# Performance work log

Measured on AMD Instinct MI355X. Metric: run time of the kernel, lower is better.

The kernel has to match this reference:

```python
import jax, jax.numpy as jnp
import numpy as np

E = 1024
M = 6
GH = 256
FR = 16  # FiLM bottleneck r = max(16, E//64)


def setup_inputs() -> dict:
    key = jax.random.key(0)
    ks = jax.random.split(key, 32)
    n = lambda k, shape, std=0.02: jax.random.normal(k, shape, dtype=jnp.float32) * std
    inp = {
        "x": jax.random.normal(ks[0], (4, 2048, E), dtype=jnp.float32),
        # gate MLP E->GH->M
        "gw1": n(ks[1], (E, GH)), "gb1": jnp.zeros((GH,), jnp.float32),
        "gw2": n(ks[2], (GH, M)), "gb2": jnp.zeros((M,), jnp.float32),
        "ebias": jnp.zeros((M,), jnp.float32),
        "pm_alpha": jnp.float32(0.5),
        # expert 0: DoubleMLP E->2E->E
        "dfc_w": n(ks[3], (E, 2 * E)), "dfc_b": jnp.zeros((2 * E,), jnp.float32),
        "dproj_w": n(ks[4], (2 * E, E)), "dproj_b": jnp.zeros((E,), jnp.float32),
        # expert 1: SingleMLP E->E->E
        "sfc_w": n(ks[5], (E, E)), "sfc_b": jnp.zeros((E,), jnp.float32),
        "sproj_w": n(ks[6], (E, E)), "sproj_b": jnp.zeros((E,), jnp.float32),
        # expert 2: rank-2 perceptron
        "p2_w": n(ks[7], (2, E)), "p2_v": n(ks[8], (2, E)),
        "p2_alpha": jnp.ones((2,), jnp.float32), "p2_b": jnp.zeros((2,), jnp.float32),
        "p2_bias": jnp.zeros((E,), jnp.float32),
        # expert 3: rank-4 perceptron
        "p4_w": n(ks[9], (4, E)), "p4_v": n(ks[10], (4, E)),
        "p4_alpha": jnp.ones((4,), jnp.float32), "p4_b": jnp.zeros((4,), jnp.float32),
        "p4_bias": jnp.zeros((E,), jnp.float32),
        # expert 4: ReGLU1D
        "rg_u": n(ks[11], (E,)), "rg_a": jnp.ones((E,), jnp.float32),
        "rg_b": jnp.zeros((1,), jnp.float32), "rg_bias": jnp.zeros((E,), jnp.float32),
        # expert 5: FiLM E->FR->2E
        "fl_dw": n(ks[12], (E, FR)), "fl_db": jnp.zeros((FR,), jnp.float32),
        "fl_uw": n(ks[13], (FR, 2 * E)), "fl_ub": jnp.zeros((2 * E,), jnp.float32),
    }
    return inp


def _gelu(x):
    return jax.nn.gelu(x, approximate=False)  # torch nn.GELU default (erf)


def _rank_n(x, w, v, alpha, b, biasvec):
    # y = biasvec + sum_i alpha_i * gelu(<w_i,x> + b_i) * v_i
    s = jnp.einsum("bse,ne->bsn", x, w) + b
    g = _gelu(s)
    return jnp.einsum("bsn,ne->bse", alpha * g, v) + biasvec


def reference(x, gw1, gb1, gw2, gb2, ebias, pm_alpha,
              dfc_w, dfc_b, dproj_w, dproj_b,
              sfc_w, sfc_b, sproj_w, sproj_b,
              p2_w, p2_v, p2_alpha, p2_b, p2_bias,
              p4_w, p4_v, p4_alpha, p4_b, p4_bias,
              rg_u, rg_a, rg_b, rg_bias,
              fl_dw, fl_db, fl_uw, fl_ub):
    # gate logits [B,S,M]; tau=1.0
    gl = _gelu(x @ gw1 + gb1) @ gw2 + gb2 + ebias
    pi = jax.nn.softmax(gl, axis=-1)
    # top_k=1 sparse weights: mask to top-1 then renormalize
    _, topi = jax.lax.top_k(pi, 1)
    mask = jax.nn.one_hot(topi[..., 0], M, dtype=pi.dtype)
    w = pi * mask
    w = w / (jnp.sum(w, axis=-1, keepdims=True) + 1e-9)

    # experts (dropout = identity in eval)
    o0 = _gelu(x @ dfc_w + dfc_b) @ dproj_w + dproj_b            # DoubleMLP
    o1 = _gelu(x @ sfc_w + sfc_b) @ sproj_w + sproj_b            # SingleMLP
    o2 = _rank_n(x, p2_w, p2_v, p2_alpha, p2_b, p2_bias)          # perc2
    o3 = _rank_n(x, p4_w, p4_v, p4_alpha, p4_b, p4_bias)          # perc4
    s = x @ rg_u + rg_b[0]                                        # ReGLU1D
    o4 = jax.nn.sigmoid(s)[..., None] * (x * rg_a) + rg_bias
    t = _gelu(x @ fl_dw + fl_db)                                  # FiLM
    gb = t @ fl_uw + fl_ub
    gamma, beta = jnp.split(gb, 2, axis=-1)
    o5 = gamma * x + beta

    all_out = jnp.stack([o0, o1, o2, o3, o4, o5], axis=-1)        # [B,S,E,M]
    mixed = jnp.sum(all_out * w[..., None, :], axis=-1)
    return pm_alpha * mixed
```

## Files before the change

### kernel.cpp

```cpp
#include <hip/hip_runtime.h>
#include <math.h>


#define E 1024
#define GH 256
#define NEXP 6
#define NTOK 8192
#define NCH 24

typedef __attribute__((ext_vector_type(8))) short bf16x8;
typedef __attribute__((ext_vector_type(4))) float f32x4;

__device__ __forceinline__ float gelu_erf(float v) {
    return 0.5f * v * (1.0f + erff(v * 0.70710678118654752440f));
}

__device__ __forceinline__ unsigned short f2bf(float f) {
    union { float f; unsigned u; } c; c.f = f;
    unsigned u = c.u;
    u += 0x7fffu + ((u >> 16) & 1u);
    return (unsigned short)(u >> 16);
}

__device__ __forceinline__ float bf2f(unsigned short h) {
    union { unsigned u; float f; } c; c.u = ((unsigned)h) << 16;
    return c.f;
}

__device__ __forceinline__ int ldso(int row, int q) {
    return row * 32 + ((q ^ ((row >> 1) & 3)) << 3);
}

__device__ __forceinline__ void glds16(const void* g, void* l) {
    __builtin_amdgcn_global_load_lds(
        (const __attribute__((address_space(1))) void*)g,
        (__attribute__((address_space(3))) void*)l, 16, 0, 0);
}

__global__ __launch_bounds__(256)
void prep_kernel(const float* __restrict__ x, unsigned short* __restrict__ xh,
                 unsigned short* __restrict__ xl,
                 const float* __restrict__ gw1, unsigned short* __restrict__ w1cat,
                 const float* __restrict__ p2_w, const float* __restrict__ p4_w,
                 const float* __restrict__ rg_u, const float* __restrict__ fl_dw,
                 unsigned short* __restrict__ w1cheap,
                 const float* __restrict__ dfc_w, unsigned short* __restrict__ dfc_wt,
                 const float* __restrict__ dproj_w, unsigned short* __restrict__ dpj_wt,
                 const float* __restrict__ sfc_w, unsigned short* __restrict__ sfc_wt,
                 const float* __restrict__ sproj_w, unsigned short* __restrict__ spj_wt) {
    __shared__ float tile[32][33];
    const int tid = threadIdx.x;
    const int tx = tid & 31, ty = tid >> 5;
    int b = blockIdx.x;
    if (b < 2048) {
        const int n4 = NTOK * E / 4;
        for (int i = b * 256 + tid; i < n4; i += 2048 * 256) {
            float4 v = reinterpret_cast<const float4*>(x)[i];
            ushort4 h, l;
            h.x = f2bf(v.x); l.x = f2bf(v.x - bf2f(h.x));
            h.y = f2bf(v.y); l.y = f2bf(v.y - bf2f(h.y));
            h.z = f2bf(v.z); l.z = f2bf(v.z - bf2f(h.z));
            h.w = f2bf(v.w); l.w = f2bf(v.w - bf2f(h.w));
            reinterpret_cast<ushort4*>(xh)[i] = h;
            reinterpret_cast<ushort4*>(xl)[i] = l;
        }
        return;
    }
    b -= 2048;
    if (b < 256) {
        const int c0 = (b & 7) * 32, r0 = (b >> 3) * 32;
#pragma unroll
        for (int i = 0; i < 4; ++i)
            tile[ty + i * 8][tx] = gw1[(size_t)(r0 + ty + i * 8) * GH + c0 + tx];
        __syncthreads();
#pragma unroll
        for (int i = 0; i < 4; ++i) {
            float v = tile[tx][ty + i * 8];
            unsigned short h = f2bf(v);
            size_t row = (size_t)(c0 + ty + i * 8) * 2048;
            w1cat[row + r0 + tx] = h;
            w1cat[row + 1024 + r0 + tx] = f2bf(v - bf2f(h));
        }
        return;
    }
    b -= 256;
    if (b < 64) {
        const int r = b;
        const int k4 = tid * 4;
        float4 v = {0.f, 0.f, 0.f, 0.f};
        if (r < 2)       v = *reinterpret_cast<const float4*>(&p2_w[r * E + k4]);
        else if (r < 6)  v = *reinterpret_cast<const float4*>(&p4_w[(r - 2) * E + k4]);
        else if (r == 6) v = *reinterpret_cast<const float4*>(&rg_u[k4]);
        else if (r < 23) {
            const int j = r - 7;
            v.x = fl_dw[(k4 + 0) * 16 + j];
            v.y = fl_dw[(k4 + 1) * 16 + j];
            v.z = fl_dw[(k4 + 2) * 16 + j];
            v.w = fl_dw[(k4 + 3) * 16 + j];
        }
        ushort4 h, l;
        h.x = f2bf(v.x); l.x = f2bf(v.x - bf2f(h.x));
        h.y = f2bf(v.y); l.y = f2bf(v.y - bf2f(h.y));
        h.z = f2bf(v.z); l.z = f2bf(v.z - bf2f(h.z));
        h.w = f2bf(v.w); l.w = f2bf(v.w - bf2f(h.w));
        *reinterpret_cast<ushort4*>(&w1cheap[r * 2048 + k4]) = h;
        *reinterpret_cast<ushort4*>(&w1cheap[r * 2048 + 1024 + k4]) = l;
        return;
    }
    b -= 64;
    const float* src; unsigned short* dst; int R, C, nbx;
    if (b < 2048)      { src = dfc_w;   dst = dfc_wt; R = 1024; C = 2048; nbx = 64; }
    else if (b < 4096) { src = dproj_w; dst = dpj_wt; R = 2048; C = 1024; nbx = 32; b -= 2048; }
    else if (b < 5120) { src = sfc_w;   dst = sfc_wt; R = 1024; C = 1024; nbx = 32; b -= 4096; }
    else               { src = sproj_w; dst = spj_wt; R = 1024; C = 1024; nbx = 32; b -= 5120; }
    const int c0 = (b % nbx) * 32, r0 = (b / nbx) * 32;
#pragma unroll
    for (int i = 0; i < 4; ++i)
        tile[ty + i * 8][tx] = src[(size_t)(r0 + ty + i * 8) * C + c0 + tx];
    __syncthreads();
#pragma unroll
    for (int i = 0; i < 4; ++i)
        dst[(size_t)(c0 + ty + i * 8) * R + r0 + tx] = f2bf(tile[tx][ty + i * 8]);
}

__global__ __launch_bounds__(256)
void gate_partial_kernel(const unsigned short* __restrict__ xh,
                         const unsigned short* __restrict__ xl,
                         const unsigned short* __restrict__ w1cat,
                         const unsigned short* __restrict__ w1cheap,
                         float* __restrict__ hp,
                         float* __restrict__ cdot) {
    __shared__ __align__(16) unsigned short As[2][128 * 32];
    __shared__ __align__(16) unsigned short Bs[2][128 * 32];
    const int tid = threadIdx.x;
    const int bid = blockIdx.x;
    const int xcd = bid & 7, slot = bid >> 3;
    const int nx = slot & 1;
    const int strip = xcd * 32 + (slot >> 1);
    const int m = strip >> 2, c2 = strip & 3;
    const int z = c2 & 1, h = c2 >> 1;
    const int t0 = m * 128, n0 = nx * 128;
    const unsigned short* A = z ? xl : xh;
    float* hpz = hp + (size_t)c2 * ((size_t)NTOK * GH);
    float* cd  = cdot + (size_t)c2 * ((size_t)NTOK * NCH);

    const int lane = tid & 63, wv = tid >> 6;
    const int wr = wv >> 1, wc = wv & 1;
    const int lm = lane & 15, q = lane >> 4;
    const int r0 = tid >> 2, gsl = tid & 3;
    const int g = gsl ^ ((r0 >> 1) & 3);
    const int lbase = wv * 512;

    const unsigned short* pa0 = A + (size_t)(t0 + r0) * E + g * 8;
    const unsigned short* pa1 = A + (size_t)(t0 + 64 + r0) * E + g * 8;
    const unsigned short* pb0 = w1cat + (size_t)(n0 + r0) * 2048 + h * 1024 + g * 8;
    const unsigned short* pb1 = w1cat + (size_t)(n0 + 64 + r0) * 2048 + h * 1024 + g * 8;
    const unsigned short* pcw = w1cheap + (size_t)(nx * 16 + lm) * 2048 + h * 1024 + q * 8;

    f32x4 acc[4][4];
#pragma unroll
    for (int s = 0; s < 4; ++s)
#pragma unroll
        for (int t = 0; t < 4; ++t) acc[s][t] = (f32x4){0.f, 0.f, 0.f, 0.f};
    f32x4 accC[2];
    accC[0] = (f32x4){0.f, 0.f, 0.f, 0.f};
    accC[1] = (f32x4){0.f, 0.f, 0.f, 0.f};

    glds16(pa0, &As[0][lbase]);
    glds16(pa1, &As[0][2048 + lbase]);
    glds16(pb0, &Bs[0][lbase]);
    glds16(pb1, &Bs[0][2048 + lbase]);
    bf16x8 cfv = *(const bf16x8*)pcw;

    int cur = 0;
    for (int k0 = 0;; k0 += 32) {
        __syncthreads();
        const int kn = k0 + 32;
        bf16x8 cfn;
        if (kn < 1024) {
            glds16(pa0 + kn, &As[cur ^ 1][lbase]);
            glds16(pa1 + kn, &As[cur ^ 1][2048 + lbase]);
            glds16(pb0 + kn, &Bs[cur ^ 1][lbase]);
            glds16(pb1 + kn, &Bs[cur ^ 1][2048 + lbase]);
            cfn = *(const bf16x8*)(pcw + kn);
        }
        bf16x8 af[4], bfr[4];
#pragma unroll
        for (int s = 0; s < 4; ++s) af[s] = *(const bf16x8*)&As[cur][ldso(wr * 64 + s * 16 + lm, q)];
#pragma unroll
        for (int t = 0; t < 4; ++t) bfr[t] = *(const bf16x8*)&Bs[cur][ldso(wc * 64 + t * 16 + lm, q)];
#pragma unroll
        for (int s = 0; s < 4; ++s)
#pragma unroll
            for (int t = 0; t < 4; ++t)
                acc[s][t] = __builtin_amdgcn_mfma_f32_16x16x32_bf16(af[s], bfr[t], acc[s][t], 0, 0, 0);
        {
            bf16x8 ac0 = wc ? af[2] : af[0];
            bf16x8 ac1 = wc ? af[3] : af[1];
            accC[0] = __builtin_amdgcn_mfma_f32_16x16x32_bf16(ac0, cfv, accC[0], 0, 0, 0);
            accC[1] = __builtin_amdgcn_mfma_f32_16x16x32_bf16(ac1, cfv, accC[1], 0, 0, 0);
        }
        if (kn >= 1024) break;
        cfv = cfn; cur ^= 1;
    }
#pragma unroll
    for (int s = 0; s < 4; ++s)
#pragma unroll
        for (int t = 0; t < 4; ++t)
#pragma unroll
            for (int rg = 0; rg < 4; ++rg) {
                int rl = wr * 64 + s * 16 + q * 4 + rg;
                int c  = wc * 64 + t * 16 + lm;
                hpz[(size_t)(t0 + rl) * GH + n0 + c] = acc[s][t][rg];
            }
    const int cc = nx * 16 + lm;
    if (cc < NCH) {
#pragma unroll
        for (int i = 0; i < 2; ++i)
#pragma unroll
            for (int rg = 0; rg < 4; ++rg) {
                int rl = wr * 64 + wc * 32 + i * 16 + q * 4 + rg;
                cd[(size_t)(t0 + rl) * NCH + cc] = accC[i][rg];
            }
    }
}

__global__ __launch_bounds__(256)
void gate_finalize_kernel(const float* __restrict__ hp,
                          const float* __restrict__ gb1, const float* __restrict__ gw2,
                          const float* __restrict__ gb2, const float* __restrict__ ebias,
                          const float* __restrict__ pm_alpha,
                          const float* __restrict__ cdot,
                          const float* __restrict__ p2_alpha, const float* __restrict__ p2_b,
                          const float* __restrict__ p4_alpha, const float* __restrict__ p4_b,
                          const float* __restrict__ rg_b, const float* __restrict__ fl_db,
                          float* __restrict__ scale, int* __restrict__ counts,
                          int* __restrict__ tlist, int* __restrict__ eid,
                          float* __restrict__ gvec) {
    __shared__ float hs[32][264];
    __shared__ float g2s[GH * NEXP];
    __shared__ int tokexp[32];
    const int tid = threadIdx.x;
    const int t0 = blockIdx.x * 32;
    const size_t HPS = (size_t)NTOK * GH;
    for (int i = tid; i < GH * NEXP; i += 256) g2s[i] = gw2[i];
#pragma unroll
    for (int i = 0; i < 8; ++i) {
        int f4 = i * 256 + tid;
        int row = f4 >> 6, c4 = (f4 & 63) * 4;
        size_t base = (size_t)(t0 + row) * GH + c4;
        float4 a = *reinterpret_cast<const float4*>(&hp[base]);
        float4 b = *reinterpret_cast<const float4*>(&hp[HPS + base]);
        float4 c = *reinterpret_cast<const float4*>(&hp[2 * HPS + base]);
        float4 d = *reinterpret_cast<const float4*>(&hp[3 * HPS + base]);
        float4 o;
        o.x = gelu_erf(a.x + b.x + c.x + d.x + gb1[c4 + 0]);
        o.y = gelu_erf(a.y + b.y + c.y + d.y + gb1[c4 + 1]);
        o.z = gelu_erf(a.z + b.z + c.z + d.z + gb1[c4 + 2]);
        o.w = gelu_erf(a.w + b.w + c.w + d.w + gb1[c4 + 3]);
        *reinterpret_cast<float4*>(&hs[row][c4]) = o;
    }
    __syncthreads();
    const int t = tid >> 3, j = tid & 7;
    float p[NEXP] = {0.f, 0.f, 0.f, 0.f, 0.f, 0.f};
#pragma unroll 8
    for (int kk = 0; kk < 32; ++kk) {
        int k = j + kk * 8;
        float hv = hs[t][k];
        const float* gr = &g2s[k * NEXP];
#pragma unroll
        for (int m = 0; m < NEXP; ++m) p[m] += hv * gr[m];
    }
#pragma unroll
    for (int m = 0; m < NEXP; ++m) {
        p[m] += __shfl_xor(p[m], 4, 64);
        p[m] += __shfl_xor(p[m], 2, 64);
        p[m] += __shfl_xor(p[m], 1, 64);
    }
    if (j == 0) {
        float L[NEXP];
#pragma unroll
        for (int m = 0; m < NEXP; ++m) L[m] = p[m] + gb2[m] + ebias[m];
        float mx = L[0]; int am = 0;
#pragma unroll
        for (int m = 1; m < NEXP; ++m) { if (L[m] > mx) { mx = L[m]; am = m; } }
        float S = 0.f;
#pragma unroll
        for (int m = 0; m < NEXP; ++m) S += expf(L[m] - mx);
        float pt = 1.f / S;
        scale[t0 + t] = pm_alpha[0] * (pt / (pt + 1e-9f));
        eid[t0 + t] = am;
        tokexp[t] = am;
    }
    __syncthreads();
    if (tid < NEXP) {
        const int e = tid;
        int cnt = 0;
#pragma unroll
        for (int i = 0; i < 32; ++i) cnt += (tokexp[i] == e);
        if (cnt) {
            int base = atomicAdd(&counts[e], cnt);
            int pos = 0;
#pragma unroll
            for (int i = 0; i < 32; ++i)
                if (tokexp[i] == e) tlist[e * NTOK + base + (pos++)] = t0 + i;
        }
    }
    const size_t CDS = (size_t)NTOK * NCH;
    for (int i = tid; i < 32 * NCH; i += 256) {
        const int tt = i / NCH, slot = i - tt * NCH;
        const int tok = t0 + tt;
        size_t idx = (size_t)tok * NCH + slot;
        float s = cdot[idx] + cdot[CDS + idx] + cdot[2 * CDS + idx] + cdot[3 * CDS + idx];
        float val;
        if (slot < 2)       val = p2_alpha[slot] * gelu_erf(s + p2_b[slot]);
        else if (slot < 6)  val = p4_alpha[slot - 2] * gelu_erf(s + p4_b[slot - 2]);
        else if (slot == 6) val = 1.f / (1.f + expf(-(s + rg_b[0])));
        else if (slot < 23) val = gelu_erf(s + fl_db[slot - 7]);
        else                val = 0.f;
        gvec[(size_t)tok * NCH + slot] = val;
    }
}

__global__ __launch_bounds__(256)
void moe_gemm1_kernel(const unsigned short* __restrict__ xh,
                      const unsigned short* __restrict__ B0, const unsigned short* __restrict__ B1,
                      const float* __restrict__ bias0, const float* __restrict__ bias1,
                      const int* __restrict__ counts, const int* __restrict__ tlist,
                      unsigned short* __restrict__ H0, unsigned short* __restrict__ H1) {
    __shared__ __align__(16) unsigned short As[2][128 * 32];
    __shared__ __align__(16) unsigned short Bs[2][128 * 32];
    __shared__ int toks[128];
    const int tid = threadIdx.x;
    const int bid = blockIdx.x;
    const int xcd = bid & 7, slot = bid >> 3;
    int z, l, nx;
    if (slot < 32) { z = 0; l = slot >> 4; nx = slot & 15; }
    else           { z = 1; l = (slot - 32) >> 3; nx = (slot - 32) & 7; }
    const int mtile = xcd + 8 * l;
    const int i0 = mtile * 128, n0 = nx * 128;
    const int N = z ? 1024 : 2048;
    const int cnt = counts[z];
    if (i0 >= cnt) return;
    const unsigned short* Bz = z ? B1 : B0;
    const float* bias = z ? bias1 : bias0;

    if (tid < 128) toks[tid] = tlist[z * NTOK + min(i0 + tid, cnt - 1)];
    __syncthreads();

    const int lane = tid & 63, wv = tid >> 6;
    const int wr = wv >> 1, wc = wv & 1;
    const int lm = lane & 15, q = lane >> 4;
    const int r0 = tid >> 2, gsl = tid & 3;
    const int g = gsl ^ ((r0 >> 1) & 3);
    const int lbase = wv * 512;

    const unsigned short* pa0 = xh + (size_t)toks[r0] * E + g * 8;
    const unsigned short* pa1 = xh + (size_t)toks[64 + r0] * E + g * 8;
    const unsigned short* pb0 = Bz + (size_t)(n0 + r0) * E + g * 8;
    const unsigned short* pb1 = Bz + (size_t)(n0 + 64 + r0) * E + g * 8;

    f32x4 acc[4][4];
#pragma unroll
    for (int s = 0; s < 4; ++s)
#pragma unroll
        for (int t = 0; t < 4; ++t) acc[s][t] = (f32x4){0.f, 0.f, 0.f, 0.f};

    glds16(pa0, &As[0][lbase]);
    glds16(pa1, &As[0][2048 + lbase]);
    glds16(pb0, &Bs[0][lbase]);
    glds16(pb1, &Bs[0][2048 + lbase]);

    int cur = 0;
    for (int k0 = 0;; k0 += 32) {
        __syncthreads();
        const int kn = k0 + 32;
        if (kn < E) {
            glds16(pa0 + kn, &As[cur ^ 1][lbase]);
            glds16(pa1 + kn, &As[cur ^ 1][2048 + lbase]);
            glds16(pb0 + kn, &Bs[cur ^ 1][lbase]);
            glds16(pb1 + kn, &Bs[cur ^ 1][2048 + lbase]);
        }
        bf16x8 af[4], bfr[4];
#pragma unroll
        for (int s = 0; s < 4; ++s) af[s] = *(const bf16x8*)&As[cur][ldso(wr * 64 + s * 16 + lm, q)];
#pragma unroll
        for (int t = 0; t < 4; ++t) bfr[t] = *(const bf16x8*)&Bs[cur][ldso(wc * 64 + t * 16 + lm, q)];
#pragma unroll
        for (int s = 0; s < 4; ++s)
#pragma unroll
            for (int t = 0; t < 4; ++t)
                acc[s][t] = __builtin_amdgcn_mfma_f32_16x16x32_bf16(af[s], bfr[t], acc[s][t], 0, 0, 0);
        if (kn >= E) break;
        cur ^= 1;
    }
    unsigned short* Hz = z ? H1 : H0;
#pragma unroll
    for (int s = 0; s < 4; ++s)
#pragma unroll
        for (int t = 0; t < 4; ++t)
#pragma unroll
            for (int rg = 0; rg < 4; ++rg) {
                int rl = wr * 64 + s * 16 + q * 4 + rg;
                int gc = n0 + wc * 64 + t * 16 + lm;
                float v = acc[s][t][rg] + bias[gc];
                Hz[(size_t)(i0 + rl) * N + gc] = f2bf(gelu_erf(v));
            }
}

__global__ __launch_bounds__(256)
void gemm2_cheap_kernel(const unsigned short* __restrict__ h1, const unsigned short* __restrict__ h2,
                        const unsigned short* __restrict__ dpj, const unsigned short* __restrict__ spj,
                        const float* __restrict__ dproj_b, const float* __restrict__ sproj_b,
                        const int* __restrict__ counts, const int* __restrict__ tlist,
                        const float* __restrict__ scale,
                        const float* __restrict__ x, const int* __restrict__ eid,
                        const float* __restrict__ gvec,
                        const float* __restrict__ p2_v, const float* __restrict__ p2_bias,
                        const float* __restrict__ p4_v, const float* __restrict__ p4_bias,
                        const float* __restrict__ rg_a, const float* __restrict__ rg_bias,
                        const float* __restrict__ fl_uw, const float* __restrict__ fl_ub,
                        float* __restrict__ out) {
    __shared__ __align__(16) unsigned short As[2][128 * 32];
    __shared__ __align__(16) unsigned short Bs[2][128 * 32];
    __shared__ int toks[128];
    const int tid = threadIdx.x;
    const int bb = blockIdx.x;
    const int lane = tid & 63;

    if (bb < 256) {
        const int xcd = bb & 7, slot = bb >> 3;
        const int z = slot >> 4;
        const int s2 = slot & 15;
        const int l = s2 >> 3, nx = s2 & 7;
        const int mtile = xcd + 8 * l;
        const int i0 = mtile * 128, n0 = nx * 128;
        const int K = z ? 1024 : 2048;
        const int cnt = counts[z];
        if (i0 >= cnt) return;
        const int rows = min(128, cnt - i0);
        const unsigned short* Az = z ? h2 : h1;
        const unsigned short* Bz = z ? spj : dpj;
        const float* bias = z ? sproj_b : dproj_b;

        if (tid < 128) toks[tid] = tlist[z * NTOK + min(i0 + tid, cnt - 1)];
        __syncthreads();

        const int wv = tid >> 6;
        const int wr = wv >> 1, wc = wv & 1;
        const int lm = lane & 15, q = lane >> 4;
        const int r0 = tid >> 2, gsl = tid & 3;
        const int g = gsl ^ ((r0 >> 1) & 3);
        const int lbase = wv * 512;

        const unsigned short* pa0 = Az + (size_t)(i0 + r0) * K + g * 8;
        const unsigned short* pa1 = Az + (size_t)(i0 + 64 + r0) * K + g * 8;
        const unsigned short* pb0 = Bz + (size_t)(n0 + r0) * K + g * 8;
        const unsigned short* pb1 = Bz + (size_t)(n0 + 64 + r0) * K + g * 8;

        f32x4 acc[4][4];
#pragma unroll
        for (int s = 0; s < 4; ++s)
#pragma unroll
            for (int t = 0; t < 4; ++t) acc[s][t] = (f32x4){0.f, 0.f, 0.f, 0.f};

        glds16(pa0, &As[0][lbase]);
        glds16(pa1, &As[0][2048 + lbase]);
        glds16(pb0, &Bs[0][lbase]);
        glds16(pb1, &Bs[0][2048 + lbase]);

        int cur = 0;
        for (int k0 = 0;; k0 += 32) {
            __syncthreads();
            const int kn = k0 + 32;
            if (kn < K) {
                glds16(pa0 + kn, &As[cur ^ 1][lbase]);
                glds16(pa1 + kn, &As[cur ^ 1][2048 + lbase]);
                glds16(pb0 + kn, &Bs[cur ^ 1][lbase]);
                glds16(pb1 + kn, &Bs[cur ^ 1][2048 + lbase]);
            }
            bf16x8 af[4], bfr[4];
#pragma unroll
            for (int s = 0; s < 4; ++s) af[s] = *(const bf16x8*)&As[cur][ldso(wr * 64 + s * 16 + lm, q)];
#pragma unroll
            for (int t = 0; t < 4; ++t) bfr[t] = *(const bf16x8*)&Bs[cur][ldso(wc * 64 + t * 16 + lm, q)];
#pragma unroll
            for (int s = 0; s < 4; ++s)
#pragma unroll
                for (int t = 0; t < 4; ++t)
                    acc[s][t] = __builtin_amdgcn_mfma_f32_16x16x32_bf16(af[s], bfr[t], acc[s][t], 0, 0, 0);
            if (kn >= K) break;
            cur ^= 1;
        }
#pragma unroll
        for (int s = 0; s < 4; ++s)
#pragma unroll
            for (int t = 0; t < 4; ++t)
#pragma unroll
                for (int rg = 0; rg < 4; ++rg) {
                    int rl = wr * 64 + s * 16 + q * 4 + rg;
                    if (rl < rows) {
                        int gc = n0 + wc * 64 + t * 16 + lm;
                        int tok = toks[rl];
                        out[(size_t)tok * E + gc] = scale[tok] * (acc[s][t][rg] + bias[gc]);
                    }
                }
        return;
    }

    const int tok = bb - 256;
    const int e = eid[tok];
    if (e < 2) return;
    const float sc = scale[tok];
    const int k4 = tid * 4;
    const float* gv = &gvec[(size_t)tok * NCH];
    float4 o;

    if (e == 2) {
        const float g0 = gv[0], g1 = gv[1];
        float4 b0 = *reinterpret_cast<const float4*>(&p2_bias[k4]);
        float4 v0 = *reinterpret_cast<const float4*>(&p2_v[k4]);
        float4 v1 = *reinterpret_cast<const float4*>(&p2_v[E + k4]);
        o.x = b0.x + g0 * v0.x + g1 * v1.x;
        o.y = b0.y + g0 * v0.y + g1 * v1.y;
        o.z = b0.z + g0 * v0.z + g1 * v1.z;
        o.w = b0.w + g0 * v0.w + g1 * v1.w;
    } else if (e == 3) {
        o = *reinterpret_cast<const float4*>(&p4_bias[k4]);
#pragma unroll
        for (int j = 0; j < 4; ++j) {
            const float gj = gv[2 + j];
            float4 vv = *reinterpret_cast<const float4*>(&p4_v[j * E + k4]);
            o.x += gj * vv.x; o.y += gj * vv.y; o.z += gj * vv.z; o.w += gj * vv.w;
        }
    } else if (e == 4) {
        const float sg = gv[6];
        float4 xv = *reinterpret_cast<const float4*>(&x[(size_t)tok * E + k4]);
        float4 av = *reinterpret_cast<const float4*>(&rg_a[k4]);
        float4 bv = *reinterpret_cast<const float4*>(&rg_bias[k4]);
        o.x = sg * xv.x * av.x + bv.x;
        o.y = sg * xv.y * av.y + bv.y;
        o.z = sg * xv.z * av.z + bv.z;
        o.w = sg * xv.w * av.w + bv.w;
    } else {
        float4 xv = *reinterpret_cast<const float4*>(&x[(size_t)tok * E + k4]);
        float4 ga = *reinterpret_cast<const float4*>(&fl_ub[k4]);
        float4 be = *reinterpret_cast<const float4*>(&fl_ub[E + k4]);
#pragma unroll
        for (int j = 0; j < 16; ++j) {
            const float tj = gv[7 + j];
            float4 ug = *reinterpret_cast<const float4*>(&fl_uw[(size_t)j * 2 * E + k4]);
            float4 ub = *reinterpret_cast<const float4*>(&fl_uw[(size_t)j * 2 * E + E + k4]);
            ga.x += tj * ug.x; ga.y += tj * ug.y; ga.z += tj * ug.z; ga.w += tj * ug.w;
            be.x += tj * ub.x; be.y += tj * ub.y; be.z += tj * ub.z; be.w += tj * ub.w;
        }
        o.x = ga.x * xv.x + be.x;
        o.y = ga.y * xv.y + be.y;
        o.z = ga.z * xv.z + be.z;
        o.w = ga.w * xv.w + be.w;
    }
    o.x *= sc; o.y *= sc; o.z *= sc; o.w *= sc;
    *reinterpret_cast<float4*>(&out[(size_t)tok * E + k4]) = o;
}

extern "C" void kernel_launch(void* const* d_in, const int* in_sizes, int n_in,
                              void* d_out, int out_size, void* d_ws, size_t ws_size,
                              hipStream_t stream) {
    const float* x        = (const float*)d_in[0];
    const float* gw1      = (const float*)d_in[1];
    const float* gb1      = (const float*)d_in[2];
    const float* gw2      = (const float*)d_in[3];
    const float* gb2      = (const float*)d_in[4];
    const float* ebias    = (const float*)d_in[5];
    const float* pm_alpha = (const float*)d_in[6];
    const float* dfc_w    = (const float*)d_in[7];
    const float* dfc_b    = (const float*)d_in[8];
    const float* dproj_w  = (const float*)d_in[9];
    const float* dproj_b  = (const float*)d_in[10];
    const float* sfc_w    = (const float*)d_in[11];
    const float* sfc_b    = (const float*)d_in[12];
    const float* sproj_w  = (const float*)d_in[13];
    const float* sproj_b  = (const float*)d_in[14];
    const float* p2_w     = (const float*)d_in[15];
    const float* p2_v     = (const float*)d_in[16];
    const float* p2_alpha = (const float*)d_in[17];
    const float* p2_b     = (const float*)d_in[18];
    const float* p2_bias  = (const float*)d_in[19];
    const float* p4_w     = (const float*)d_in[20];
    const float* p4_v     = (const float*)d_in[21];
    const float* p4_alpha = (const float*)d_in[22];
    const float* p4_b     = (const float*)d_in[23];
    const float* p4_bias  = (const float*)d_in[24];
    const float* rg_u     = (const float*)d_in[25];
    const float* rg_a     = (const float*)d_in[26];
    const float* rg_b     = (const float*)d_in[27];
    const float* rg_bias  = (const float*)d_in[28];
    const float* fl_dw    = (const float*)d_in[29];
    const float* fl_db    = (const float*)d_in[30];
    const float* fl_uw    = (const float*)d_in[31];
    const float* fl_ub    = (const float*)d_in[32];
    float* out = (float*)d_out;

    char* ws = (char*)d_ws;
    size_t off = 0;
    int*            counts = (int*)(ws + off);            off += 256;
    float*          scale  = (float*)(ws + off);          off += (size_t)NTOK * 4;
    int*            tlist  = (int*)(ws + off);            off += (size_t)NEXP * NTOK * 4;
    int*            eid    = (int*)(ws + off);            off += (size_t)NTOK * 4;
    float*          gvec   = (float*)(ws + off);          off += (size_t)NTOK * NCH * 4;
    float*          cdot   = (float*)(ws + off);          off += (size_t)4 * NTOK * NCH * 4;
    unsigned short* w1cheap= (unsigned short*)(ws + off); off += (size_t)64 * 2048 * 2;
    unsigned short* w1cat  = (unsigned short*)(ws + off); off += (size_t)GH * 2048 * 2;
    unsigned short* dfc_wt = (unsigned short*)(ws + off); off += (size_t)2048 * 1024 * 2;
    unsigned short* dpj_wt = (unsigned short*)(ws + off); off += (size_t)1024 * 2048 * 2;
    unsigned short* sfc_wt = (unsigned short*)(ws + off); off += (size_t)1024 * 1024 * 2;
    unsigned short* spj_wt = (unsigned short*)(ws + off); off += (size_t)1024 * 1024 * 2;
    unsigned short* x_hi   = (unsigned short*)(ws + off); off += (size_t)NTOK * E * 2;
    char* U = ws + off;
    unsigned short* x_lo = (unsigned short*)U;
    unsigned short* h1   = (unsigned short*)U;
    unsigned short* h2   = (unsigned short*)(U + (size_t)16 * 1024 * 1024);
    float* hp = out;

    hipMemsetAsync(counts, 0, 256, stream);
    prep_kernel<<<8512, 256, 0, stream>>>(x, x_hi, x_lo, gw1, w1cat,
                                          p2_w, p4_w, rg_u, fl_dw, w1cheap,
                                          dfc_w, dfc_wt, dproj_w, dpj_wt,
                                          sfc_w, sfc_wt, sproj_w, spj_wt);
    gate_partial_kernel<<<512, 256, 0, stream>>>(
        x_hi, x_lo, w1cat, w1cheap, hp, cdot);
    gate_finalize_kernel<<<NTOK / 32, 256, 0, stream>>>(
        hp, gb1, gw2, gb2, ebias, pm_alpha, cdot,
        p2_alpha, p2_b, p4_alpha, p4_b, rg_b, fl_db,
        scale, counts, tlist, eid, gvec);
    moe_gemm1_kernel<<<384, 256, 0, stream>>>(
        x_hi, dfc_wt, sfc_wt, dfc_b, sfc_b, counts, tlist, h1, h2);
    gemm2_cheap_kernel<<<256 + NTOK, 256, 0, stream>>>(
        h1, h2, dpj_wt, spj_wt, dproj_b, sproj_b, counts, tlist, scale,
        x, eid, gvec,
        p2_v, p2_bias, p4_v, p4_bias,
        rg_a, rg_bias, fl_uw, fl_ub, out);
    (void)in_sizes; (void)n_in; (void)out_size; (void)ws_size;
}
```

Measured before the change: 305.6 us.

## Split cheap experts into separate kernel batching tokens per expert list

Separates the fused gemm2-plus-cheap-expert launch into a dedicated GEMM2 kernel and a new cheap-expert kernel. The cheap kernel walks per-expert token lists in groups of 8, loading the expert weight vectors once per group and reusing them across tokens instead of reloading them for every token. It also replaces 8192 per-token blocks, most of which exited early, with a 2048-block grid-stride loop. The cost is an extra kernel launch, and the cheap experts now run after GEMM2 instead of alongside it, so overlap between them is lost.

```diff
diff --git a/kernel.cpp b/kernel.cpp
--- a/kernel.cpp
+++ b/kernel.cpp
@@ -409,18 +409,12 @@
 }
 
 __global__ __launch_bounds__(256)
-void gemm2_cheap_kernel(const unsigned short* __restrict__ h1, const unsigned short* __restrict__ h2,
-                        const unsigned short* __restrict__ dpj, const unsigned short* __restrict__ spj,
-                        const float* __restrict__ dproj_b, const float* __restrict__ sproj_b,
-                        const int* __restrict__ counts, const int* __restrict__ tlist,
-                        const float* __restrict__ scale,
-                        const float* __restrict__ x, const int* __restrict__ eid,
-                        const float* __restrict__ gvec,
-                        const float* __restrict__ p2_v, const float* __restrict__ p2_bias,
-                        const float* __restrict__ p4_v, const float* __restrict__ p4_bias,
-                        const float* __restrict__ rg_a, const float* __restrict__ rg_bias,
-                        const float* __restrict__ fl_uw, const float* __restrict__ fl_ub,
-                        float* __restrict__ out) {
+void moe_gemm2_kernel(const unsigned short* __restrict__ h1, const unsigned short* __restrict__ h2,
+                      const unsigned short* __restrict__ dpj, const unsigned short* __restrict__ spj,
+                      const float* __restrict__ dproj_b, const float* __restrict__ sproj_b,
+                      const int* __restrict__ counts, const int* __restrict__ tlist,
+                      const float* __restrict__ scale,
+                      float* __restrict__ out) {
     __shared__ __align__(16) unsigned short As[2][128 * 32];
     __shared__ __align__(16) unsigned short Bs[2][128 * 32];
     __shared__ int toks[128];
@@ -428,139 +422,202 @@
     const int bb = blockIdx.x;
     const int lane = tid & 63;
 
-    if (bb < 256) {
-        const int xcd = bb & 7, slot = bb >> 3;
-        const int z = slot >> 4;
-        const int s2 = slot & 15;
-        const int l = s2 >> 3, nx = s2 & 7;
-        const int mtile = xcd + 8 * l;
-        const int i0 = mtile * 128, n0 = nx * 128;
-        const int K = z ? 1024 : 2048;
-        const int cnt = counts[z];
-        if (i0 >= cnt) return;
-        const int rows = min(128, cnt - i0);
-        const unsigned short* Az = z ? h2 : h1;
-        const unsigned short* Bz = z ? spj : dpj;
-        const float* bias = z ? sproj_b : dproj_b;
-
-        if (tid < 128) toks[tid] = tlist[z * NTOK + min(i0 + tid, cnt - 1)];
+    const int xcd = bb & 7, slot = bb >> 3;
+    const int z = slot >> 4;
+    const int s2 = slot & 15;
+    const int l = s2 >> 3, nx = s2 & 7;
+    const int mtile = xcd + 8 * l;
+    const int i0 = mtile * 128, n0 = nx * 128;
+    const int K = z ? 1024 : 2048;
+    const int cnt = counts[z];
+    if (i0 >= cnt) return;
+    const int rows = min(128, cnt - i0);
+    const unsigned short* Az = z ? h2 : h1;
+    const unsigned short* Bz = z ? spj : dpj;
+    const float* bias = z ? sproj_b : dproj_b;
+
+    if (tid < 128) toks[tid] = tlist[z * NTOK + min(i0 + tid, cnt - 1)];
+    __syncthreads();
+
+    const int wv = tid >> 6;
+    const int wr = wv >> 1, wc = wv & 1;
+    const int lm = lane & 15, q = lane >> 4;
+    const int r0 = tid >> 2, gsl = tid & 3;
+    const int g = gsl ^ ((r0 >> 1) & 3);
+    const int lbase = wv * 512;
+
+    const unsigned short* pa0 = Az + (size_t)(i0 + r0) * K + g * 8;
+    const unsigned short* pa1 = Az + (size_t)(i0 + 64 + r0) * K + g * 8;
+    const unsigned short* pb0 = Bz + (size_t)(n0 + r0) * K + g * 8;
+    const unsigned short* pb1 = Bz + (size_t)(n0 + 64 + r0) * K + g * 8;
+
+    f32x4 acc[4][4];
+#pragma unroll
+    for (int s = 0; s < 4; ++s)
+#pragma unroll
+        for (int t = 0; t < 4; ++t) acc[s][t] = (f32x4){0.f, 0.f, 0.f, 0.f};
+
+    glds16(pa0, &As[0][lbase]);
+    glds16(pa1, &As[0][2048 + lbase]);
+    glds16(pb0, &Bs[0][lbase]);
+    glds16(pb1, &Bs[0][2048 + lbase]);
+
+    int cur = 0;
+    for (int k0 = 0;; k0 += 32) {
         __syncthreads();
-
-        const int wv = tid >> 6;
-        const int wr = wv >> 1, wc = wv & 1;
-        const int lm = lane & 15, q = lane >> 4;
-        const int r0 = tid >> 2, gsl = tid & 3;
-        const int g = gsl ^ ((r0 >> 1) & 3);
-        const int lbase = wv * 512;
-
-        const unsigned short* pa0 = Az + (size_t)(i0 + r0) * K + g * 8;
-        const unsigned short* pa1 = Az + (size_t)(i0 + 64 + r0) * K + g * 8;
-        const unsigned short* pb0 = Bz + (size_t)(n0 + r0) * K + g * 8;
-        const unsigned short* pb1 = Bz + (size_t)(n0 + 64 + r0) * K + g * 8;
-
-        f32x4 acc[4][4];
+        const int kn = k0 + 32;
+        if (kn < K) {
+            glds16(pa0 + kn, &As[cur ^ 1][lbase]);
+            glds16(pa1 + kn, &As[cur ^ 1][2048 + lbase]);
+            glds16(pb0 + kn, &Bs[cur ^ 1][lbase]);
+            glds16(pb1 + kn, &Bs[cur ^ 1][2048 + lbase]);
+        }
+        bf16x8 af[4], bfr[4];
+#pragma unroll
+        for (int s = 0; s < 4; ++s) af[s] = *(const bf16x8*)&As[cur][ldso(wr * 64 + s * 16 + lm, q)];
+#pragma unroll
+        for (int t = 0; t < 4; ++t) bfr[t] = *(const bf16x8*)&Bs[cur][ldso(wc * 64 + t * 16 + lm, q)];
 #pragma unroll
         for (int s = 0; s < 4; ++s)
 #pragma unroll
-            for (int t = 0; t < 4; ++t) acc[s][t] = (f32x4){0.f, 0.f, 0.f, 0.f};
-
-        glds16(pa0, &As[0][lbase]);
-        glds16(pa1, &As[0][2048 + lbase]);
-        glds16(pb0, &Bs[0][lbase]);
-        glds16(pb1, &Bs[0][2048 + lbase]);
-
-        int cur = 0;
-        for (int k0 = 0;; k0 += 32) {
-            __syncthreads();
-            const int kn = k0 + 32;
-            if (kn < K) {
-                glds16(pa0 + kn, &As[cur ^ 1][lbase]);
-                glds16(pa1 + kn, &As[cur ^ 1][2048 + lbase]);
-                glds16(pb0 + kn, &Bs[cur ^ 1][lbase]);
-                glds16(pb1 + kn, &Bs[cur ^ 1][2048 + lbase]);
-            }
-            bf16x8 af[4], bfr[4];
-#pragma unroll
-            for (int s = 0; s < 4; ++s) af[s] = *(const bf16x8*)&As[cur][ldso(wr * 64 + s * 16 + lm, q)];
-#pragma unroll
-            for (int t = 0; t < 4; ++t) bfr[t] = *(const bf16x8*)&Bs[cur][ldso(wc * 64 + t * 16 + lm, q)];
-#pragma unroll
-            for (int s = 0; s < 4; ++s)
-#pragma unroll
-                for (int t = 0; t < 4; ++t)
-                    acc[s][t] = __builtin_amdgcn_mfma_f32_16x16x32_bf16(af[s], bfr[t], acc[s][t], 0, 0, 0);
-            if (kn >= K) break;
-            cur ^= 1;
-        }
-#pragma unroll
-        for (int s = 0; s < 4; ++s)
-#pragma unroll
             for (int t = 0; t < 4; ++t)
-#pragma unroll
-                for (int rg = 0; rg < 4; ++rg) {
-                    int rl = wr * 64 + s * 16 + q * 4 + rg;
-                    if (rl < rows) {
-                        int gc = n0 + wc * 64 + t * 16 + lm;
-                        int tok = toks[rl];
-                        out[(size_t)tok * E + gc] = scale[tok] * (acc[s][t][rg] + bias[gc]);
+                acc[s][t] = __builtin_amdgcn_mfma_f32_16x16x32_bf16(af[s], bfr[t], acc[s][t], 0, 0, 0);
+        if (kn >= K) break;
+        cur ^= 1;
+    }
+#pragma unroll
+    for (int s = 0; s < 4; ++s)
+#pragma unroll
+        for (int t = 0; t < 4; ++t)
+#pragma unroll
+            for (int rg = 0; rg < 4; ++rg) {
+                int rl = wr * 64 + s * 16 + q * 4 + rg;
+                if (rl < rows) {
+                    int gc = n0 + wc * 64 + t * 16 + lm;
+                    int tok = toks[rl];
+                    out[(size_t)tok * E + gc] = scale[tok] * (acc[s][t][rg] + bias[gc]);
+                }
+            }
+}
+
+__global__ __launch_bounds__(256)
+void cheap_kernel(const int* __restrict__ counts, const int* __restrict__ tlist,
+                  const float* __restrict__ scale, const float* __restrict__ x,
+                  const float* __restrict__ gvec,
+                  const float* __restrict__ p2_v, const float* __restrict__ p2_bias,
+                  const float* __restrict__ p4_v, const float* __restrict__ p4_bias,
+                  const float* __restrict__ rg_a, const float* __restrict__ rg_bias,
+                  const float* __restrict__ fl_uw, const float* __restrict__ fl_ub,
+                  float* __restrict__ out) {
+    __shared__ int stoks[8];
+    __shared__ float ssc[8];
+    __shared__ float sgv[8][17];
+    const int tid = threadIdx.x;
+    const int k4 = tid * 4;
+    for (int s = blockIdx.x; s < 4096; s += 2048) {
+        const int e = 2 + (s & 3);
+        const int ti = s >> 2;
+        const int cnt = counts[e];
+        const int i0 = ti * 8;
+        if (i0 >= cnt) continue;
+        const int nt = min(8, cnt - i0);
+        __syncthreads();
+        if (tid < 128) {
+            const int tt = tid >> 4, sl = tid & 15;
+            const int tk = tlist[e * NTOK + min(i0 + tt, cnt - 1)];
+            if (sl == 0) { stoks[tt] = tk; ssc[tt] = scale[tk]; }
+            const int base = (e == 2) ? 0 : (e == 3) ? 2 : (e == 4) ? 6 : 7;
+            const int ng   = (e == 2) ? 2 : (e == 3) ? 4 : (e == 4) ? 1 : 16;
+            if (sl < ng) sgv[tt][sl] = gvec[(size_t)tk * NCH + base + sl];
+        }
+        __syncthreads();
+        if (e == 2) {
+            const float4 b0 = *reinterpret_cast<const float4*>(&p2_bias[k4]);
+            const float4 v0 = *reinterpret_cast<const float4*>(&p2_v[k4]);
+            const float4 v1 = *reinterpret_cast<const float4*>(&p2_v[E + k4]);
+#pragma unroll
+            for (int tt = 0; tt < 8; ++tt) {
+                if (tt < nt) {
+                    const float g0 = sgv[tt][0], g1 = sgv[tt][1], sc = ssc[tt];
+                    float4 o;
+                    o.x = (b0.x + g0 * v0.x + g1 * v1.x) * sc;
+                    o.y = (b0.y + g0 * v0.y + g1 * v1.y) * sc;
+                    o.z = (b0.z + g0 * v0.z + g1 * v1.z) * sc;
+                    o.w = (b0.w + g0 * v0.w + g1 * v1.w) * sc;
+                    *reinterpret_cast<float4*>(&out[(size_t)stoks[tt] * E + k4]) = o;
+                }
+            }
+        } else if (e == 3) {
+            const float4 b0 = *reinterpret_cast<const float4*>(&p4_bias[k4]);
+            float4 vv[4];
+#pragma unroll
+            for (int j = 0; j < 4; ++j)
+                vv[j] = *reinterpret_cast<const float4*>(&p4_v[j * E + k4]);
+#pragma unroll
+            for (int tt = 0; tt < 8; ++tt) {
+                if (tt < nt) {
+                    float4 o = b0;
+#pragma unroll
+                    for (int j = 0; j < 4; ++j) {
+                        const float gj = sgv[tt][j];
+                        o.x += gj * vv[j].x; o.y += gj * vv[j].y;
+                        o.z += gj * vv[j].z; o.w += gj * vv[j].w;
                     }
+                    const float sc = ssc[tt];
+                    o.x *= sc; o.y *= sc; o.z *= sc; o.w *= sc;
+                    *reinterpret_cast<float4*>(&out[(size_t)stoks[tt] * E + k4]) = o;
                 }
-        return;
-    }
-
-    const int tok = bb - 256;
-    const int e = eid[tok];
-    if (e < 2) return;
-    const float sc = scale[tok];
-    const int k4 = tid * 4;
-    const float* gv = &gvec[(size_t)tok * NCH];
-    float4 o;
-
-    if (e == 2) {
-        const float g0 = gv[0], g1 = gv[1];
-        float4 b0 = *reinterpret_cast<const float4*>(&p2_bias[k4]);
-        float4 v0 = *reinterpret_cast<const float4*>(&p2_v[k4]);
-        float4 v1 = *reinterpret_cast<const float4*>(&p2_v[E + k4]);
-        o.x = b0.x + g0 * v0.x + g1 * v1.x;
-        o.y = b0.y + g0 * v0.y + g1 * v1.y;
-        o.z = b0.z + g0 * v0.z + g1 * v1.z;
-        o.w = b0.w + g0 * v0.w + g1 * v1.w;
-    } else if (e == 3) {
-        o = *reinterpret_cast<const float4*>(&p4_bias[k4]);
-#pragma unroll
-        for (int j = 0; j < 4; ++j) {
-            const float gj = gv[2 + j];
-            float4 vv = *reinterpret_cast<const float4*>(&p4_v[j * E + k4]);
-            o.x += gj * vv.x; o.y += gj * vv.y; o.z += gj * vv.z; o.w += gj * vv.w;
-        }
-    } else if (e == 4) {
-        const float sg = gv[6];
-        float4 xv = *reinterpret_cast<const float4*>(&x[(size_t)tok * E + k4]);
-        float4 av = *reinterpret_cast<const float4*>(&rg_a[k4]);
-        float4 bv = *reinterpret_cast<const float4*>(&rg_bias[k4]);
-        o.x = sg * xv.x * av.x + bv.x;
-        o.y = sg * xv.y * av.y + bv.y;
-        o.z = sg * xv.z * av.z + bv.z;
-        o.w = sg * xv.w * av.w + bv.w;
-    } else {
-        float4 xv = *reinterpret_cast<const float4*>(&x[(size_t)tok * E + k4]);
-        float4 ga = *reinterpret_cast<const float4*>(&fl_ub[k4]);
-        float4 be = *reinterpret_cast<const float4*>(&fl_ub[E + k4]);
-#pragma unroll
-        for (int j = 0; j < 16; ++j) {
-            const float tj = gv[7 + j];
-            float4 ug = *reinterpret_cast<const float4*>(&fl_uw[(size_t)j * 2 * E + k4]);
-            float4 ub = *reinterpret_cast<const float4*>(&fl_uw[(size_t)j * 2 * E + E + k4]);
-            ga.x += tj * ug.x; ga.y += tj * ug.y; ga.z += tj * ug.z; ga.w += tj * ug.w;
-            be.x += tj * ub.x; be.y += tj * ub.y; be.z += tj * ub.z; be.w += tj * ub.w;
-        }
-        o.x = ga.x * xv.x + be.x;
-        o.y = ga.y * xv.y + be.y;
-        o.z = ga.z * xv.z + be.z;
-        o.w = ga.w * xv.w + be.w;
-    }
-    o.x *= sc; o.y *= sc; o.z *= sc; o.w *= sc;
-    *reinterpret_cast<float4*>(&out[(size_t)tok * E + k4]) = o;
+            }
+        } else if (e == 4) {
+            const float4 av = *reinterpret_cast<const float4*>(&rg_a[k4]);
+            const float4 bv = *reinterpret_cast<const float4*>(&rg_bias[k4]);
+#pragma unroll
+            for (int tt = 0; tt < 8; ++tt) {
+                if (tt < nt) {
+                    const float sg = sgv[tt][0], sc = ssc[tt];
+                    const float4 xv = *reinterpret_cast<const float4*>(&x[(size_t)stoks[tt] * E + k4]);
+                    float4 o;
+                    o.x = (sg * xv.x * av.x + bv.x) * sc;
+                    o.y = (sg * xv.y * av.y + bv.y) * sc;
+                    o.z = (sg * xv.z * av.z + bv.z) * sc;
+                    o.w = (sg * xv.w * av.w + bv.w) * sc;
+                    *reinterpret_cast<float4*>(&out[(size_t)stoks[tt] * E + k4]) = o;
+                }
+            }
+        } else {
+            float4 ga[8], be[8];
+            const float4 g0 = *reinterpret_cast<const float4*>(&fl_ub[k4]);
+            const float4 b0 = *reinterpret_cast<const float4*>(&fl_ub[E + k4]);
+#pragma unroll
+            for (int tt = 0; tt < 8; ++tt) { ga[tt] = g0; be[tt] = b0; }
+#pragma unroll
+            for (int j = 0; j < 16; ++j) {
+                const float4 ug = *reinterpret_cast<const float4*>(&fl_uw[(size_t)j * 2 * E + k4]);
+                const float4 ub = *reinterpret_cast<const float4*>(&fl_uw[(size_t)j * 2 * E + E + k4]);
+#pragma unroll
+                for (int tt = 0; tt < 8; ++tt) {
+                    const float tj = sgv[tt][j];
+                    ga[tt].x += tj * ug.x; ga[tt].y += tj * ug.y;
+                    ga[tt].z += tj * ug.z; ga[tt].w += tj * ug.w;
+                    be[tt].x += tj * ub.x; be[tt].y += tj * ub.y;
+                    be[tt].z += tj * ub.z; be[tt].w += tj * ub.w;
+                }
+            }
+#pragma unroll
+            for (int tt = 0; tt < 8; ++tt) {
+                if (tt < nt) {
+                    const float sc = ssc[tt];
+                    const float4 xv = *reinterpret_cast<const float4*>(&x[(size_t)stoks[tt] * E + k4]);
+                    float4 o;
+                    o.x = (ga[tt].x * xv.x + be[tt].x) * sc;
+                    o.y = (ga[tt].y * xv.y + be[tt].y) * sc;
+                    o.z = (ga[tt].z * xv.z + be[tt].z) * sc;
+                    o.w = (ga[tt].w * xv.w + be[tt].w) * sc;
+                    *reinterpret_cast<float4*>(&out[(size_t)stoks[tt] * E + k4]) = o;
+                }
+            }
+        }
+    }
 }
 
 extern "C" void kernel_launch(void* const* d_in, const int* in_sizes, int n_in,
@@ -635,9 +692,10 @@
         scale, counts, tlist, eid, gvec);
     moe_gemm1_kernel<<<384, 256, 0, stream>>>(
         x_hi, dfc_wt, sfc_wt, dfc_b, sfc_b, counts, tlist, h1, h2);
-    gemm2_cheap_kernel<<<256 + NTOK, 256, 0, stream>>>(
-        h1, h2, dpj_wt, spj_wt, dproj_b, sproj_b, counts, tlist, scale,
-        x, eid, gvec,
+    moe_gemm2_kernel<<<256, 256, 0, stream>>>(
+        h1, h2, dpj_wt, spj_wt, dproj_b, sproj_b, counts, tlist, scale, out);
+    cheap_kernel<<<2048, 256, 0, stream>>>(
+        counts, tlist, scale, x, gvec,
         p2_v, p2_bias, p4_v, p4_bias,
         rg_a, rg_bias, fl_uw, fl_ub, out);
     (void)in_sizes; (void)n_in; (void)out_size; (void)ws_size;
```

Measured after the change: 330.3 us. 8.1% more time.
